# Optimization experiments

Hardware: AMD Instinct MI355X
Metric: run time of the kernel (lower is better)

The kernel has to match this reference:

```python
import jax, jax.numpy as jnp
import numpy as np

N = 2048      # nodes: 8 sequences x 256 tokens
E = 524288    # edges: dense attention graph, 8 * 256^2
H = 8         # heads
DK = 64       # per-head dim


def setup_inputs() -> dict:
    key = jax.random.key(0)
    k1, k2, k3, k4, k5 = jax.random.split(key, 5)
    q = jax.random.normal(k1, (N, H, DK), dtype=jnp.float32)
    k = jax.random.normal(k2, (N, H, DK), dtype=jnp.float32)
    v = jax.random.normal(k3, (N, H, DK), dtype=jnp.float32)
    edge_src = jax.random.randint(k4, (E,), 0, N, dtype=jnp.int32)
    edge_dst = jax.random.randint(k5, (E,), 0, N, dtype=jnp.int32)
    return {"q": q, "k": k, "v": v, "edge_src": edge_src, "edge_dst": edge_dst}


def reference(q, k, v, edge_src, edge_dst):
    # src_dot_dst('k','q','score'): per-edge dot product over head dim -> [E, H]
    score = jnp.einsum('ehd,ehd->eh', k[edge_src], q[edge_dst])
    # scaled_exp('score', sqrt(d_k)): exp(clamp(score / sqrt(d_k), -10, 10))
    score = jnp.exp(jnp.clip(score / jnp.sqrt(jnp.float32(DK)), -10.0, 10.0))
    # send_and_recv: wv = sum_dst(v_src * score), z = sum_dst(score)
    wv = jax.ops.segment_sum(v[edge_src] * score[:, :, None], edge_dst, num_segments=N)  # [N, H, DK]
    z = jax.ops.segment_sum(score, edge_dst, num_segments=N)  # [N, H]
    # post_func normalization: attention output per node
    return wv / z[:, :, None]
```

## Files before the change

kernel.cpp:

```cpp
#include <hip/hip_runtime.h>

#define NNODES 2048
#define NHEAD 8
#define DKDIM 64

typedef unsigned int uint;
typedef unsigned short ushort;
typedef unsigned char uchar;
typedef __fp16 h2 __attribute__((ext_vector_type(2)));
typedef __fp16 h8 __attribute__((ext_vector_type(8)));
typedef float f16v __attribute__((ext_vector_type(16)));

#define KSCALE 0.18033688011112042f
#define CLAMP2 14.426950408889634f

__device__ __forceinline__ uint pk2(float a, float b) {
    union { h2 h; uint u; } x; x.h = __builtin_amdgcn_cvt_pkrtz(a, b); return x.u;
}

__global__ void prep12(const float* __restrict__ k, const float* __restrict__ v,
                       uint4* __restrict__ kc4, uint4* __restrict__ vt4,
                       uint4* __restrict__ A4) {
    __shared__ float tile[64][65];
    int b = blockIdx.x, t = threadIdx.x;
    if (b < 512) {
        int i = b * 256 + t;
        int f = i >> 6, l = i & 63;
        int jq = f & 3, sr = (f >> 2) & 1, ts = (f >> 3) & 31, h = f >> 8;
        int node = ts * 64 + sr * 32 + (l & 31);
        int dim0 = (2 * jq + (l >> 5)) * 8;
        const float* src = k + (size_t)node * 512 + h * 64 + dim0;
        float4 f0 = *(const float4*)src;
        float4 f1 = *(const float4*)(src + 4);
        uint4 o;
        o.x = pk2(f0.x * KSCALE, f0.y * KSCALE);
        o.y = pk2(f0.z * KSCALE, f0.w * KSCALE);
        o.z = pk2(f1.x * KSCALE, f1.y * KSCALE);
        o.w = pk2(f1.z * KSCALE, f1.w * KSCALE);
        kc4[(size_t)f * 64 + l] = o;
    } else if (b < 768) {
        int bv = b - 512;
        int h = bv & 7, tn = bv >> 3;
        int nl = t >> 2, dq = (t & 3) * 16;
        const float* src = v + (size_t)(tn * 64 + nl) * 512 + h * 64 + dq;
#pragma unroll
        for (int i = 0; i < 4; ++i) {
            float4 f = *(const float4*)(src + i * 4);
            tile[nl][dq + i * 4 + 0] = f.x;
            tile[nl][dq + i * 4 + 1] = f.y;
            tile[nl][dq + i * 4 + 2] = f.z;
            tile[nl][dq + i * 4 + 3] = f.w;
        }
        __syncthreads();
#pragma unroll
        for (int rep = 0; rep < 2; ++rep) {
            int slot = rep * 256 + t;
            int fsub = slot >> 6, l = slot & 63;
            int srv = fsub >> 2, ks = (fsub >> 1) & 1, dg = fsub & 1;
            int dim = dg * 32 + (l & 31);
            int s8 = (srv * 4 + ks * 2 + (l >> 5)) * 8;
            uint4 o;
            o.x = pk2(tile[s8 + 0][dim], tile[s8 + 1][dim]);
            o.y = pk2(tile[s8 + 2][dim], tile[s8 + 3][dim]);
            o.z = pk2(tile[s8 + 4][dim], tile[s8 + 5][dim]);
            o.w = pk2(tile[s8 + 6][dim], tile[s8 + 7][dim]);
            int fV = (h * 32 + tn) * 8 + srv * 4 + ks * 2 + dg;
            vt4[(size_t)fV * 64 + l] = o;
        }
    } else {
        uint4 zz = {0u, 0u, 0u, 0u};
        A4[(size_t)(b - 768) * 512 + t] = zz;
        A4[(size_t)(b - 768) * 512 + t + 256] = zz;
    }
}

__global__ void histA(const int* __restrict__ es, const int* __restrict__ ed,
                      uint* __restrict__ A32, int E) {
    int i = blockIdx.x * 256 + threadIdx.x;
    if (i < E) {
        uint s = (uint)es[i], d = (uint)ed[i];
        uint uidx = ((d >> 6) << 14) + ((s >> 6) << 9) + (((s >> 5) & 1u) << 8) +
                    (((d >> 5) & 1u) << 7) + ((d & 31u) << 2) + ((s >> 3) & 3u);
        atomicAdd(&A32[uidx], 1u << ((s & 7u) << 2));
    }
}

__global__ void __launch_bounds__(512, 2) attn_kernel(
    const float* __restrict__ q, const char* __restrict__ kc, const char* __restrict__ vt,
    const uchar* __restrict__ A8, float* __restrict__ out) {
    __shared__ float CL[64 * 68];
    __shared__ float CLz[64];

    int b = blockIdx.x;
    int j = b & 7, idx = b >> 3;
    int dt = (j & 3) * 8 + (idx >> 2);
    int h = (j >> 2) * 4 + (idx & 3);
    int dst0 = dt * 64;
    int t = threadIdx.x;
    int w = t >> 6, half = w >> 2;
    int u = w & 3, sr = u >> 1, dc = u & 1;
    int l = t & 63, lm = l & 31, hi = l >> 5;

    int ts0 = half * 16;
    const char* kBase = kc + ((size_t)(h * 32 + ts0) * 8 + sr * 4) * 1024 + l * 16;
    const char* vBase = vt + ((size_t)(h * 32 + ts0) * 8 + sr * 4) * 1024 + l * 16;
    const char* aRow = (const char*)A8 + (size_t)dt * 65536 + (size_t)ts0 * 2048 +
                       sr * 1024 + dc * 512 + lm * 16;

    h8 qf[4];
    {
        const float* qp = q + (size_t)(dst0 + dc * 32 + lm) * 512 + h * 64 + hi * 8;
#pragma unroll
        for (int jq = 0; jq < 4; ++jq) {
            float4 f0 = *(const float4*)(qp + jq * 16);
            float4 f1 = *(const float4*)(qp + jq * 16 + 4);
            union { uint u4[4]; h8 v; } U;
            U.u4[0] = pk2(f0.x, f0.y); U.u4[1] = pk2(f0.z, f0.w);
            U.u4[2] = pk2(f1.x, f1.y); U.u4[3] = pk2(f1.z, f1.w);
            qf[jq] = U.v;
        }
    }

    f16v of[2];
#pragma unroll
    for (int dg = 0; dg < 2; ++dg)
#pragma unroll
        for (int i = 0; i < 16; ++i) of[dg][i] = 0.f;
    float z = 0.f;

    uint4 k0f[4], k1f[4], v0f[4], v1f[4];
    uint4 ac0, ac1;

#pragma unroll
    for (int f = 0; f < 4; ++f) {
        k0f[f] = *(const uint4*)(kBase + f * 1024);
        k1f[f] = *(const uint4*)(kBase + 8192 + f * 1024);
    }
    ac0 = *(const uint4*)aRow;
    ac1 = *(const uint4*)(aRow + 2048);

    for (int p = 0; p < 8; ++p) {
        int r0t = 2 * p, r1t = 2 * p + 1;
        size_t o0 = (size_t)r0t * 8192, o1 = (size_t)r1t * 8192;
#pragma unroll
        for (int f = 0; f < 4; ++f) {
            v0f[f] = *(const uint4*)(vBase + o0 + f * 1024);
            v1f[f] = *(const uint4*)(vBase + o1 + f * 1024);
        }

        f16v sacc0, sacc1;
#pragma unroll
        for (int i = 0; i < 16; ++i) { sacc0[i] = 0.f; sacc1[i] = 0.f; }
        __builtin_amdgcn_s_setprio(1);
#pragma unroll
        for (int jq = 0; jq < 4; ++jq) {
            union { uint4 u; h8 v; } KF; KF.u = k0f[jq];
            sacc0 = __builtin_amdgcn_mfma_f32_32x32x16_f16(KF.v, qf[jq], sacc0, 0, 0, 0);
        }
#pragma unroll
        for (int jq = 0; jq < 4; ++jq) {
            union { uint4 u; h8 v; } KF; KF.u = k1f[jq];
            sacc1 = __builtin_amdgcn_mfma_f32_32x32x16_f16(KF.v, qf[jq], sacc1, 0, 0, 0);
        }
        __builtin_amdgcn_s_setprio(0);

        int n0 = (p < 7) ? r0t + 2 : r0t;
        int n1 = (p < 7) ? r1t + 2 : r1t;
#pragma unroll
        for (int f = 0; f < 4; ++f) {
            k0f[f] = *(const uint4*)(kBase + (size_t)n0 * 8192 + f * 1024);
            k1f[f] = *(const uint4*)(kBase + (size_t)n1 * 8192 + f * 1024);
        }

        uint W0[4][2], W1[4][2];
        {
            const uint* a0 = (const uint*)&ac0;
            const uint* a1 = (const uint*)&ac1;
#pragma unroll
            for (int G = 0; G < 4; ++G) {
                float e0[4], e1[4];
#pragma unroll
                for (int j2 = 0; j2 < 4; ++j2) {
                    float s0 = fminf(fmaxf(sacc0[4 * G + j2], -CLAMP2), CLAMP2);
                    float s1 = fminf(fmaxf(sacc1[4 * G + j2], -CLAMP2), CLAMP2);
                    e0[j2] = exp2f(s0) * (float)((a0[G] >> (16 * hi + 4 * j2)) & 15u);
                    e1[j2] = exp2f(s1) * (float)((a1[G] >> (16 * hi + 4 * j2)) & 15u);
                    z += e0[j2] + e1[j2];
                }
                W0[G][0] = pk2(e0[0], e0[1]); W0[G][1] = pk2(e0[2], e0[3]);
                W1[G][0] = pk2(e1[0], e1[1]); W1[G][1] = pk2(e1[2], e1[3]);
            }
        }

        ac0 = *(const uint4*)(aRow + (size_t)n0 * 2048);
        ac1 = *(const uint4*)(aRow + (size_t)n1 * 2048);

        uint Wx0[4][2], Wx1[4][2];
#pragma unroll
        for (int G = 0; G < 4; ++G) {
            Wx0[G][0] = __shfl_xor(W0[G][0], 32);
            Wx0[G][1] = __shfl_xor(W0[G][1], 32);
            Wx1[G][0] = __shfl_xor(W1[G][0], 32);
            Wx1[G][1] = __shfl_xor(W1[G][1], 32);
        }

        __builtin_amdgcn_s_setprio(1);
#pragma unroll
        for (int ks = 0; ks < 2; ++ks) {
            union { uint u4[4]; h8 v; } S0, S1;
            S0.u4[0] = hi ? Wx0[2 * ks + 1][0] : W0[2 * ks][0];
            S0.u4[1] = hi ? Wx0[2 * ks + 1][1] : W0[2 * ks][1];
            S0.u4[2] = hi ? W0[2 * ks + 1][0] : Wx0[2 * ks][0];
            S0.u4[3] = hi ? W0[2 * ks + 1][1] : Wx0[2 * ks][1];
            S1.u4[0] = hi ? Wx1[2 * ks + 1][0] : W1[2 * ks][0];
            S1.u4[1] = hi ? Wx1[2 * ks + 1][1] : W1[2 * ks][1];
            S1.u4[2] = hi ? W1[2 * ks + 1][0] : Wx1[2 * ks][0];
            S1.u4[3] = hi ? W1[2 * ks + 1][1] : Wx1[2 * ks][1];
#pragma unroll
            for (int dg = 0; dg < 2; ++dg) {
                union { uint4 u; h8 v; } VF0, VF1;
                VF0.u = v0f[ks * 2 + dg];
                VF1.u = v1f[ks * 2 + dg];
                of[dg] = __builtin_amdgcn_mfma_f32_32x32x16_f16(VF0.v, S0.v, of[dg], 0, 0, 0);
                of[dg] = __builtin_amdgcn_mfma_f32_32x32x16_f16(VF1.v, S1.v, of[dg], 0, 0, 0);
            }
        }
        __builtin_amdgcn_s_setprio(0);
    }

    z += __shfl_xor(z, 32);

    int gid = half * 2 + sr;
    for (int p = 0; p < 4; ++p) {
        if (gid == p) {
#pragma unroll
            for (int dg = 0; dg < 2; ++dg)
#pragma unroll
                for (int reg = 0; reg < 16; ++reg) {
                    int dim = dg * 32 + (reg & 3) + 8 * (reg >> 2) + 4 * hi;
                    int idx2 = (dc * 32 + lm) * 68 + dim;
                    if (p == 0) CL[idx2] = of[dg][reg];
                    else CL[idx2] += of[dg][reg];
                }
            if (hi == 0) {
                if (p == 0) CLz[dc * 32 + lm] = z;
                else CLz[dc * 32 + lm] += z;
            }
        }
        __syncthreads();
    }

    {
        int dst = t >> 3, d8 = t & 7;
        float inv = 1.0f / CLz[dst];
        float4 o0 = *(float4*)(CL + dst * 68 + d8 * 8);
        float4 o1 = *(float4*)(CL + dst * 68 + d8 * 8 + 4);
        o0.x *= inv; o0.y *= inv; o0.z *= inv; o0.w *= inv;
        o1.x *= inv; o1.y *= inv; o1.z *= inv; o1.w *= inv;
        float* op = out + (size_t)(dst0 + dst) * 512 + h * 64 + d8 * 8;
        *(float4*)op = o0;
        *(float4*)(op + 4) = o1;
    }
}


extern "C" void kernel_launch(void* const* d_in, const int* in_sizes, int n_in,
                              void* d_out, int out_size, void* d_ws, size_t ws_size,
                              hipStream_t stream) {
    const float* q = (const float*)d_in[0];
    const float* k = (const float*)d_in[1];
    const float* v = (const float*)d_in[2];
    const int* esrc = (const int*)d_in[3];
    const int* edst = (const int*)d_in[4];
    float* out = (float*)d_out;
    const int E = in_sizes[3];

    uchar* A8 = (uchar*)d_ws;
    char* kc = (char*)(A8 + (size_t)NNODES * NNODES / 2);
    char* vt = kc + (size_t)NHEAD * NNODES * DKDIM * 2;

    prep12<<<1024, 256, 0, stream>>>(k, v, (uint4*)kc, (uint4*)vt, (uint4*)A8);
    histA<<<(E + 255) / 256, 256, 0, stream>>>(esrc, edst, (uint*)A8, E);
    attn_kernel<<<256, 512, 0, stream>>>(q, kc, vt, A8, out);
}
```

Baseline: 55.45 us.

## Fuse prep, histogram, and attention into one cooperative kernel with grid syncs

Merges the three separate launches (K/V conversion plus adjacency zeroing, edge histogram, attention) into one cooperative kernel of 256 blocks x 512 threads. Grid-wide syncs separate the phases. The aim is to remove per-launch overhead and the gaps between kernels. In exchange, the prep and histogram phases now run on only 256 blocks with more work per thread, and grid.sync adds barrier cost. The attention path is unchanged.

```diff
diff --git a/kernel.cpp b/kernel.cpp
--- a/kernel.cpp
+++ b/kernel.cpp
@@ -1,4 +1,7 @@
 #include <hip/hip_runtime.h>
+#include <hip/hip_cooperative_groups.h>
+
+namespace cg = cooperative_groups;
 
 #define NNODES 2048
 #define NHEAD 8
@@ -18,13 +21,19 @@
     union { h2 h; uint u; } x; x.h = __builtin_amdgcn_cvt_pkrtz(a, b); return x.u;
 }
 
-__global__ void prep12(const float* __restrict__ k, const float* __restrict__ v,
-                       uint4* __restrict__ kc4, uint4* __restrict__ vt4,
-                       uint4* __restrict__ A4) {
-    __shared__ float tile[64][65];
-    int b = blockIdx.x, t = threadIdx.x;
-    if (b < 512) {
-        int i = b * 256 + t;
+__global__ void __launch_bounds__(512, 2) fused_kernel(
+    const float* __restrict__ q, const float* __restrict__ k, const float* __restrict__ v,
+    const int* __restrict__ es, const int* __restrict__ ed,
+    char* __restrict__ kc, char* __restrict__ vt, uchar* __restrict__ A8,
+    float* __restrict__ out, int E) {
+    cg::grid_group grid = cg::this_grid();
+    __shared__ float shmem[64 * 68 + 64];
+
+    int bid = blockIdx.x;
+    int t = threadIdx.x;
+
+    {
+        int i = bid * 512 + t;
         int f = i >> 6, l = i & 63;
         int jq = f & 3, sr = (f >> 2) & 1, ts = (f >> 3) & 31, h = f >> 8;
         int node = ts * 64 + sr * 32 + (l & 31);
@@ -37,229 +46,231 @@
         o.y = pk2(f0.z * KSCALE, f0.w * KSCALE);
         o.z = pk2(f1.x * KSCALE, f1.y * KSCALE);
         o.w = pk2(f1.z * KSCALE, f1.w * KSCALE);
-        kc4[(size_t)f * 64 + l] = o;
-    } else if (b < 768) {
-        int bv = b - 512;
-        int h = bv & 7, tn = bv >> 3;
-        int nl = t >> 2, dq = (t & 3) * 16;
+        ((uint4*)kc)[(size_t)f * 64 + l] = o;
+    }
+
+    {
+        float (*tile)[65] = (float (*)[65])shmem;
+        int h = bid & 7, tn = bid >> 3;
+        int nl = t >> 3, dq = (t & 7) * 8;
         const float* src = v + (size_t)(tn * 64 + nl) * 512 + h * 64 + dq;
-#pragma unroll
-        for (int i = 0; i < 4; ++i) {
-            float4 f = *(const float4*)(src + i * 4);
-            tile[nl][dq + i * 4 + 0] = f.x;
-            tile[nl][dq + i * 4 + 1] = f.y;
-            tile[nl][dq + i * 4 + 2] = f.z;
-            tile[nl][dq + i * 4 + 3] = f.w;
-        }
+        float4 f0 = *(const float4*)src;
+        float4 f1 = *(const float4*)(src + 4);
+        tile[nl][dq + 0] = f0.x; tile[nl][dq + 1] = f0.y;
+        tile[nl][dq + 2] = f0.z; tile[nl][dq + 3] = f0.w;
+        tile[nl][dq + 4] = f1.x; tile[nl][dq + 5] = f1.y;
+        tile[nl][dq + 6] = f1.z; tile[nl][dq + 7] = f1.w;
         __syncthreads();
-#pragma unroll
-        for (int rep = 0; rep < 2; ++rep) {
-            int slot = rep * 256 + t;
-            int fsub = slot >> 6, l = slot & 63;
-            int srv = fsub >> 2, ks = (fsub >> 1) & 1, dg = fsub & 1;
-            int dim = dg * 32 + (l & 31);
-            int s8 = (srv * 4 + ks * 2 + (l >> 5)) * 8;
-            uint4 o;
-            o.x = pk2(tile[s8 + 0][dim], tile[s8 + 1][dim]);
-            o.y = pk2(tile[s8 + 2][dim], tile[s8 + 3][dim]);
-            o.z = pk2(tile[s8 + 4][dim], tile[s8 + 5][dim]);
-            o.w = pk2(tile[s8 + 6][dim], tile[s8 + 7][dim]);
-            int fV = (h * 32 + tn) * 8 + srv * 4 + ks * 2 + dg;
-            vt4[(size_t)fV * 64 + l] = o;
-        }
-    } else {
+        int fsub = t >> 6, l = t & 63;
+        int srv = fsub >> 2, ks = (fsub >> 1) & 1, dg = fsub & 1;
+        int dim = dg * 32 + (l & 31);
+        int s8 = (srv * 4 + ks * 2 + (l >> 5)) * 8;
+        uint4 o;
+        o.x = pk2(tile[s8 + 0][dim], tile[s8 + 1][dim]);
+        o.y = pk2(tile[s8 + 2][dim], tile[s8 + 3][dim]);
+        o.z = pk2(tile[s8 + 4][dim], tile[s8 + 5][dim]);
+        o.w = pk2(tile[s8 + 6][dim], tile[s8 + 7][dim]);
+        int fV = (h * 32 + tn) * 8 + fsub;
+        ((uint4*)vt)[(size_t)fV * 64 + l] = o;
+    }
+
+    {
         uint4 zz = {0u, 0u, 0u, 0u};
-        A4[(size_t)(b - 768) * 512 + t] = zz;
-        A4[(size_t)(b - 768) * 512 + t + 256] = zz;
-    }
-}
-
-__global__ void histA(const int* __restrict__ es, const int* __restrict__ ed,
-                      uint* __restrict__ A32, int E) {
-    int i = blockIdx.x * 256 + threadIdx.x;
-    if (i < E) {
-        uint s = (uint)es[i], d = (uint)ed[i];
-        uint uidx = ((d >> 6) << 14) + ((s >> 6) << 9) + (((s >> 5) & 1u) << 8) +
-                    (((d >> 5) & 1u) << 7) + ((d & 31u) << 2) + ((s >> 3) & 3u);
-        atomicAdd(&A32[uidx], 1u << ((s & 7u) << 2));
-    }
-}
-
-__global__ void __launch_bounds__(512, 2) attn_kernel(
-    const float* __restrict__ q, const char* __restrict__ kc, const char* __restrict__ vt,
-    const uchar* __restrict__ A8, float* __restrict__ out) {
-    __shared__ float CL[64 * 68];
-    __shared__ float CLz[64];
-
-    int b = blockIdx.x;
-    int j = b & 7, idx = b >> 3;
-    int dt = (j & 3) * 8 + (idx >> 2);
-    int h = (j >> 2) * 4 + (idx & 3);
-    int dst0 = dt * 64;
-    int t = threadIdx.x;
-    int w = t >> 6, half = w >> 2;
-    int u = w & 3, sr = u >> 1, dc = u & 1;
-    int l = t & 63, lm = l & 31, hi = l >> 5;
-
-    int ts0 = half * 16;
-    const char* kBase = kc + ((size_t)(h * 32 + ts0) * 8 + sr * 4) * 1024 + l * 16;
-    const char* vBase = vt + ((size_t)(h * 32 + ts0) * 8 + sr * 4) * 1024 + l * 16;
-    const char* aRow = (const char*)A8 + (size_t)dt * 65536 + (size_t)ts0 * 2048 +
-                       sr * 1024 + dc * 512 + lm * 16;
-
-    h8 qf[4];
-    {
-        const float* qp = q + (size_t)(dst0 + dc * 32 + lm) * 512 + h * 64 + hi * 8;
-#pragma unroll
-        for (int jq = 0; jq < 4; ++jq) {
-            float4 f0 = *(const float4*)(qp + jq * 16);
-            float4 f1 = *(const float4*)(qp + jq * 16 + 4);
-            union { uint u4[4]; h8 v; } U;
-            U.u4[0] = pk2(f0.x, f0.y); U.u4[1] = pk2(f0.z, f0.w);
-            U.u4[2] = pk2(f1.x, f1.y); U.u4[3] = pk2(f1.z, f1.w);
-            qf[jq] = U.v;
-        }
-    }
-
-    f16v of[2];
-#pragma unroll
-    for (int dg = 0; dg < 2; ++dg)
-#pragma unroll
-        for (int i = 0; i < 16; ++i) of[dg][i] = 0.f;
-    float z = 0.f;
-
-    uint4 k0f[4], k1f[4], v0f[4], v1f[4];
-    uint4 ac0, ac1;
-
-#pragma unroll
-    for (int f = 0; f < 4; ++f) {
-        k0f[f] = *(const uint4*)(kBase + f * 1024);
-        k1f[f] = *(const uint4*)(kBase + 8192 + f * 1024);
-    }
-    ac0 = *(const uint4*)aRow;
-    ac1 = *(const uint4*)(aRow + 2048);
-
-    for (int p = 0; p < 8; ++p) {
-        int r0t = 2 * p, r1t = 2 * p + 1;
-        size_t o0 = (size_t)r0t * 8192, o1 = (size_t)r1t * 8192;
+        ((uint4*)A8)[(size_t)bid * 512 + t] = zz;
+    }
+
+    grid.sync();
+
+    {
+        uint* A32 = (uint*)A8;
+#pragma unroll
+        for (int e = 0; e < 4; ++e) {
+            int i = bid * 512 + t + e * 131072;
+            if (i < E) {
+                uint s = (uint)es[i], d = (uint)ed[i];
+                uint uidx = ((d >> 6) << 14) + ((s >> 6) << 9) + (((s >> 5) & 1u) << 8) +
+                            (((d >> 5) & 1u) << 7) + ((d & 31u) << 2) + ((s >> 3) & 3u);
+                atomicAdd(&A32[uidx], 1u << ((s & 7u) << 2));
+            }
+        }
+    }
+
+    grid.sync();
+
+    {
+        float* CL = shmem;
+        float* CLz = shmem + 64 * 68;
+
+        int b = bid;
+        int j = b & 7, idx = b >> 3;
+        int dt = (j & 3) * 8 + (idx >> 2);
+        int h = (j >> 2) * 4 + (idx & 3);
+        int dst0 = dt * 64;
+        int w = t >> 6, half = w >> 2;
+        int u = w & 3, sr = u >> 1, dc = u & 1;
+        int l = t & 63, lm = l & 31, hi = l >> 5;
+
+        int ts0 = half * 16;
+        const char* kBase = kc + ((size_t)(h * 32 + ts0) * 8 + sr * 4) * 1024 + l * 16;
+        const char* vBase = vt + ((size_t)(h * 32 + ts0) * 8 + sr * 4) * 1024 + l * 16;
+        const char* aRow = (const char*)A8 + (size_t)dt * 65536 + (size_t)ts0 * 2048 +
+                           sr * 1024 + dc * 512 + lm * 16;
+
+        h8 qf[4];
+        {
+            const float* qp = q + (size_t)(dst0 + dc * 32 + lm) * 512 + h * 64 + hi * 8;
+#pragma unroll
+            for (int jq = 0; jq < 4; ++jq) {
+                float4 f0 = *(const float4*)(qp + jq * 16);
+                float4 f1 = *(const float4*)(qp + jq * 16 + 4);
+                union { uint u4[4]; h8 v; } U;
+                U.u4[0] = pk2(f0.x, f0.y); U.u4[1] = pk2(f0.z, f0.w);
+                U.u4[2] = pk2(f1.x, f1.y); U.u4[3] = pk2(f1.z, f1.w);
+                qf[jq] = U.v;
+            }
+        }
+
+        f16v of[2];
+#pragma unroll
+        for (int dg = 0; dg < 2; ++dg)
+#pragma unroll
+            for (int i = 0; i < 16; ++i) of[dg][i] = 0.f;
+        float z = 0.f;
+
+        uint4 k0f[4], k1f[4], v0f[4], v1f[4];
+        uint4 ac0, ac1;
+
 #pragma unroll
         for (int f = 0; f < 4; ++f) {
-            v0f[f] = *(const uint4*)(vBase + o0 + f * 1024);
-            v1f[f] = *(const uint4*)(vBase + o1 + f * 1024);
-        }
-
-        f16v sacc0, sacc1;
-#pragma unroll
-        for (int i = 0; i < 16; ++i) { sacc0[i] = 0.f; sacc1[i] = 0.f; }
-        __builtin_amdgcn_s_setprio(1);
-#pragma unroll
-        for (int jq = 0; jq < 4; ++jq) {
-            union { uint4 u; h8 v; } KF; KF.u = k0f[jq];
-            sacc0 = __builtin_amdgcn_mfma_f32_32x32x16_f16(KF.v, qf[jq], sacc0, 0, 0, 0);
-        }
-#pragma unroll
-        for (int jq = 0; jq < 4; ++jq) {
-            union { uint4 u; h8 v; } KF; KF.u = k1f[jq];
-            sacc1 = __builtin_amdgcn_mfma_f32_32x32x16_f16(KF.v, qf[jq], sacc1, 0, 0, 0);
-        }
-        __builtin_amdgcn_s_setprio(0);
-
-        int n0 = (p < 7) ? r0t + 2 : r0t;
-        int n1 = (p < 7) ? r1t + 2 : r1t;
-#pragma unroll
-        for (int f = 0; f < 4; ++f) {
-            k0f[f] = *(const uint4*)(kBase + (size_t)n0 * 8192 + f * 1024);
-            k1f[f] = *(const uint4*)(kBase + (size_t)n1 * 8192 + f * 1024);
-        }
-
-        uint W0[4][2], W1[4][2];
+            k0f[f] = *(const uint4*)(kBase + f * 1024);
+            k1f[f] = *(const uint4*)(kBase + 8192 + f * 1024);
+        }
+        ac0 = *(const uint4*)aRow;
+        ac1 = *(const uint4*)(aRow + 2048);
+
+        for (int p = 0; p < 8; ++p) {
+            int r0t = 2 * p, r1t = 2 * p + 1;
+            size_t o0 = (size_t)r0t * 8192, o1 = (size_t)r1t * 8192;
+#pragma unroll
+            for (int f = 0; f < 4; ++f) {
+                v0f[f] = *(const uint4*)(vBase + o0 + f * 1024);
+                v1f[f] = *(const uint4*)(vBase + o1 + f * 1024);
+            }
+
+            f16v sacc0, sacc1;
+#pragma unroll
+            for (int i = 0; i < 16; ++i) { sacc0[i] = 0.f; sacc1[i] = 0.f; }
+            __builtin_amdgcn_s_setprio(1);
+#pragma unroll
+            for (int jq = 0; jq < 4; ++jq) {
+                union { uint4 u; h8 v; } KF; KF.u = k0f[jq];
+                sacc0 = __builtin_amdgcn_mfma_f32_32x32x16_f16(KF.v, qf[jq], sacc0, 0, 0, 0);
+            }
+#pragma unroll
+            for (int jq = 0; jq < 4; ++jq) {
+                union { uint4 u; h8 v; } KF; KF.u = k1f[jq];
+                sacc1 = __builtin_amdgcn_mfma_f32_32x32x16_f16(KF.v, qf[jq], sacc1, 0, 0, 0);
+            }
+            __builtin_amdgcn_s_setprio(0);
+
+            int n0 = (p < 7) ? r0t + 2 : r0t;
+            int n1 = (p < 7) ? r1t + 2 : r1t;
+#pragma unroll
+            for (int f = 0; f < 4; ++f) {
+                k0f[f] = *(const uint4*)(kBase + (size_t)n0 * 8192 + f * 1024);
+                k1f[f] = *(const uint4*)(kBase + (size_t)n1 * 8192 + f * 1024);
+            }
+
+            uint W0[4][2], W1[4][2];
+            {
+                const uint* a0 = (const uint*)&ac0;
+                const uint* a1 = (const uint*)&ac1;
+#pragma unroll
+                for (int G = 0; G < 4; ++G) {
+                    float e0[4], e1[4];
+#pragma unroll
+                    for (int j2 = 0; j2 < 4; ++j2) {
+                        float s0 = fminf(fmaxf(sacc0[4 * G + j2], -CLAMP2), CLAMP2);
+                        float s1 = fminf(fmaxf(sacc1[4 * G + j2], -CLAMP2), CLAMP2);
+                        e0[j2] = exp2f(s0) * (float)((a0[G] >> (16 * hi + 4 * j2)) & 15u);
+                        e1[j2] = exp2f(s1) * (float)((a1[G] >> (16 * hi + 4 * j2)) & 15u);
+                        z += e0[j2] + e1[j2];
+                    }
+                    W0[G][0] = pk2(e0[0], e0[1]); W0[G][1] = pk2(e0[2], e0[3]);
+                    W1[G][0] = pk2(e1[0], e1[1]); W1[G][1] = pk2(e1[2], e1[3]);
+                }
+            }
+
+            ac0 = *(const uint4*)(aRow + (size_t)n0 * 2048);
+            ac1 = *(const uint4*)(aRow + (size_t)n1 * 2048);
+
+            uint Wx0[4][2], Wx1[4][2];
+#pragma unroll
+            for (int G = 0; G < 4; ++G) {
+                Wx0[G][0] = __shfl_xor(W0[G][0], 32);
+                Wx0[G][1] = __shfl_xor(W0[G][1], 32);
+                Wx1[G][0] = __shfl_xor(W1[G][0], 32);
+                Wx1[G][1] = __shfl_xor(W1[G][1], 32);
+            }
+
+            __builtin_amdgcn_s_setprio(1);
+#pragma unroll
+            for (int ks = 0; ks < 2; ++ks) {
+                union { uint u4[4]; h8 v; } S0, S1;
+                S0.u4[0] = hi ? Wx0[2 * ks + 1][0] : W0[2 * ks][0];
+                S0.u4[1] = hi ? Wx0[2 * ks + 1][1] : W0[2 * ks][1];
+                S0.u4[2] = hi ? W0[2 * ks + 1][0] : Wx0[2 * ks][0];
+                S0.u4[3] = hi ? W0[2 * ks + 1][1] : Wx0[2 * ks][1];
+                S1.u4[0] = hi ? Wx1[2 * ks + 1][0] : W1[2 * ks][0];
+                S1.u4[1] = hi ? Wx1[2 * ks + 1][1] : W1[2 * ks][1];
+                S1.u4[2] = hi ? W1[2 * ks + 1][0] : Wx1[2 * ks][0];
+                S1.u4[3] = hi ? W1[2 * ks + 1][1] : Wx1[2 * ks][1];
+#pragma unroll
+                for (int dg = 0; dg < 2; ++dg) {
+                    union { uint4 u; h8 v; } VF0, VF1;
+                    VF0.u = v0f[ks * 2 + dg];
+                    VF1.u = v1f[ks * 2 + dg];
+                    of[dg] = __builtin_amdgcn_mfma_f32_32x32x16_f16(VF0.v, S0.v, of[dg], 0, 0, 0);
+                    of[dg] = __builtin_amdgcn_mfma_f32_32x32x16_f16(VF1.v, S1.v, of[dg], 0, 0, 0);
+                }
+            }
+            __builtin_amdgcn_s_setprio(0);
+        }
+
+        z += __shfl_xor(z, 32);
+
+        __syncthreads();
+        int gid = half * 2 + sr;
+        for (int p = 0; p < 4; ++p) {
+            if (gid == p) {
+#pragma unroll
+                for (int dg = 0; dg < 2; ++dg)
+#pragma unroll
+                    for (int reg = 0; reg < 16; ++reg) {
+                        int dim = dg * 32 + (reg & 3) + 8 * (reg >> 2) + 4 * hi;
+                        int idx2 = (dc * 32 + lm) * 68 + dim;
+                        if (p == 0) CL[idx2] = of[dg][reg];
+                        else CL[idx2] += of[dg][reg];
+                    }
+                if (hi == 0) {
+                    if (p == 0) CLz[dc * 32 + lm] = z;
+                    else CLz[dc * 32 + lm] += z;
+                }
+            }
+            __syncthreads();
+        }
+
         {
-            const uint* a0 = (const uint*)&ac0;
-            const uint* a1 = (const uint*)&ac1;
-#pragma unroll
-            for (int G = 0; G < 4; ++G) {
-                float e0[4], e1[4];
-#pragma unroll
-                for (int j2 = 0; j2 < 4; ++j2) {
-                    float s0 = fminf(fmaxf(sacc0[4 * G + j2], -CLAMP2), CLAMP2);
-                    float s1 = fminf(fmaxf(sacc1[4 * G + j2], -CLAMP2), CLAMP2);
-                    e0[j2] = exp2f(s0) * (float)((a0[G] >> (16 * hi + 4 * j2)) & 15u);
-                    e1[j2] = exp2f(s1) * (float)((a1[G] >> (16 * hi + 4 * j2)) & 15u);
-                    z += e0[j2] + e1[j2];
-                }
-                W0[G][0] = pk2(e0[0], e0[1]); W0[G][1] = pk2(e0[2], e0[3]);
-                W1[G][0] = pk2(e1[0], e1[1]); W1[G][1] = pk2(e1[2], e1[3]);
-            }
-        }
-
-        ac0 = *(const uint4*)(aRow + (size_t)n0 * 2048);
-        ac1 = *(const uint4*)(aRow + (size_t)n1 * 2048);
-
-        uint Wx0[4][2], Wx1[4][2];
-#pragma unroll
-        for (int G = 0; G < 4; ++G) {
-            Wx0[G][0] = __shfl_xor(W0[G][0], 32);
-            Wx0[G][1] = __shfl_xor(W0[G][1], 32);
-            Wx1[G][0] = __shfl_xor(W1[G][0], 32);
-            Wx1[G][1] = __shfl_xor(W1[G][1], 32);
-        }
-
-        __builtin_amdgcn_s_setprio(1);
-#pragma unroll
-        for (int ks = 0; ks < 2; ++ks) {
-            union { uint u4[4]; h8 v; } S0, S1;
-            S0.u4[0] = hi ? Wx0[2 * ks + 1][0] : W0[2 * ks][0];
-            S0.u4[1] = hi ? Wx0[2 * ks + 1][1] : W0[2 * ks][1];
-            S0.u4[2] = hi ? W0[2 * ks + 1][0] : Wx0[2 * ks][0];
-            S0.u4[3] = hi ? W0[2 * ks + 1][1] : Wx0[2 * ks][1];
-            S1.u4[0] = hi ? Wx1[2 * ks + 1][0] : W1[2 * ks][0];
-            S1.u4[1] = hi ? Wx1[2 * ks + 1][1] : W1[2 * ks][1];
-            S1.u4[2] = hi ? W1[2 * ks + 1][0] : Wx1[2 * ks][0];
-            S1.u4[3] = hi ? W1[2 * ks + 1][1] : Wx1[2 * ks][1];
-#pragma unroll
-            for (int dg = 0; dg < 2; ++dg) {
-                union { uint4 u; h8 v; } VF0, VF1;
-                VF0.u = v0f[ks * 2 + dg];
-                VF1.u = v1f[ks * 2 + dg];
-                of[dg] = __builtin_amdgcn_mfma_f32_32x32x16_f16(VF0.v, S0.v, of[dg], 0, 0, 0);
-                of[dg] = __builtin_amdgcn_mfma_f32_32x32x16_f16(VF1.v, S1.v, of[dg], 0, 0, 0);
-            }
-        }
-        __builtin_amdgcn_s_setprio(0);
-    }
-
-    z += __shfl_xor(z, 32);
-
-    int gid = half * 2 + sr;
-    for (int p = 0; p < 4; ++p) {
-        if (gid == p) {
-#pragma unroll
-            for (int dg = 0; dg < 2; ++dg)
-#pragma unroll
-                for (int reg = 0; reg < 16; ++reg) {
-                    int dim = dg * 32 + (reg & 3) + 8 * (reg >> 2) + 4 * hi;
-                    int idx2 = (dc * 32 + lm) * 68 + dim;
-                    if (p == 0) CL[idx2] = of[dg][reg];
-                    else CL[idx2] += of[dg][reg];
-                }
-            if (hi == 0) {
-                if (p == 0) CLz[dc * 32 + lm] = z;
-                else CLz[dc * 32 + lm] += z;
-            }
-        }
-        __syncthreads();
-    }
-
-    {
-        int dst = t >> 3, d8 = t & 7;
-        float inv = 1.0f / CLz[dst];
-        float4 o0 = *(float4*)(CL + dst * 68 + d8 * 8);
-        float4 o1 = *(float4*)(CL + dst * 68 + d8 * 8 + 4);
-        o0.x *= inv; o0.y *= inv; o0.z *= inv; o0.w *= inv;
-        o1.x *= inv; o1.y *= inv; o1.z *= inv; o1.w *= inv;
-        float* op = out + (size_t)(dst0 + dst) * 512 + h * 64 + d8 * 8;
-        *(float4*)op = o0;
-        *(float4*)(op + 4) = o1;
+            int dst = t >> 3, d8 = t & 7;
+            float inv = 1.0f / CLz[dst];
+            float4 o0 = *(float4*)(CL + dst * 68 + d8 * 8);
+            float4 o1 = *(float4*)(CL + dst * 68 + d8 * 8 + 4);
+            o0.x *= inv; o0.y *= inv; o0.z *= inv; o0.w *= inv;
+            o1.x *= inv; o1.y *= inv; o1.z *= inv; o1.w *= inv;
+            float* op = out + (size_t)(dst0 + dst) * 512 + h * 64 + d8 * 8;
+            *(float4*)op = o0;
+            *(float4*)(op + 4) = o1;
+        }
     }
 }
 
@@ -273,13 +284,14 @@
     const int* esrc = (const int*)d_in[3];
     const int* edst = (const int*)d_in[4];
     float* out = (float*)d_out;
-    const int E = in_sizes[3];
+    int E = in_sizes[3];
 
     uchar* A8 = (uchar*)d_ws;
     char* kc = (char*)(A8 + (size_t)NNODES * NNODES / 2);
     char* vt = kc + (size_t)NHEAD * NNODES * DKDIM * 2;
 
-    prep12<<<1024, 256, 0, stream>>>(k, v, (uint4*)kc, (uint4*)vt, (uint4*)A8);
-    histA<<<(E + 255) / 256, 256, 0, stream>>>(esrc, edst, (uint*)A8, E);
-    attn_kernel<<<256, 512, 0, stream>>>(q, kc, vt, A8, out);
+    void* args[] = {(void*)&q, (void*)&k, (void*)&v, (void*)&esrc, (void*)&edst,
+                    (void*)&kc, (void*)&vt, (void*)&A8, (void*)&out, (void*)&E};
+    (void)hipLaunchCooperativeKernel((const void*)fused_kernel, dim3(256), dim3(512),
+                                     args, 0, stream);
 }
```

Result: slower. 121.6 us (+119.3%).
